# Optimization experiments

Measured on AMD Instinct MI355X. Metric: run time of the kernel, lower is better.

## Reference

```python
import jax, jax.numpy as jnp
import numpy as np

EPS = 1e-5

def layer_norm(x, g, b):
    m = jnp.mean(x, axis=-1, keepdims=True)
    v = jnp.var(x, axis=-1, keepdims=True)
    return (x - m) / jnp.sqrt(v + EPS) * g + b

def setup_inputs() -> dict:
    key = jax.random.key(0)
    B, N, D, H, F = 2, 2048, 1024, 16, 4096
    ks = jax.random.split(key, 12)
    s = 0.02
    return {
        "x": jax.random.normal(ks[0], (B, N, D), dtype=jnp.float32),
        "wq": jax.random.normal(ks[1], (D, D), dtype=jnp.float32) * s,
        "bq": jnp.zeros((D,), jnp.float32),
        "wk": jax.random.normal(ks[2], (D, D), dtype=jnp.float32) * s,
        "bk": jnp.zeros((D,), jnp.float32),
        "wv": jax.random.normal(ks[3], (D, D), dtype=jnp.float32) * s,
        "bv": jnp.zeros((D,), jnp.float32),
        "g1": jnp.ones((D,), jnp.float32),
        "b1": jnp.zeros((D,), jnp.float32),
        "g2": jnp.ones((D,), jnp.float32),
        "b2": jnp.zeros((D,), jnp.float32),
        "w1": jax.random.normal(ks[4], (D, F), dtype=jnp.float32) * s,
        "bw1": jnp.zeros((F,), jnp.float32),
        "gf": jnp.ones((F,), jnp.float32),
        "bf": jnp.zeros((F,), jnp.float32),
        "w2": jax.random.normal(ks[5], (F, D), dtype=jnp.float32) * s,
        "bw2": jnp.zeros((D,), jnp.float32),
        "num_heads": 16,
    }

def reference(x, wq, bq, wk, bk, wv, bv, g1, b1, g2, b2, w1, bw1, gf, bf, w2, bw2, num_heads):
    B, N, D = x.shape
    H = num_heads
    E = D // H
    h = layer_norm(x, g1, b1)
    q = (h @ wq + bq).reshape(B, N, H, E).transpose(0, 2, 1, 3)  # B H N E
    k = (h @ wk + bk).reshape(B, N, H, E).transpose(0, 2, 1, 3)
    v = (h @ wv + bv).reshape(B, N, H, E).transpose(0, 2, 1, 3)
    # NOTE: original scales by 1/sqrt(1/emb_dim) == sqrt(emb_dim)
    scale = jnp.sqrt(jnp.float32(D))
    score = jnp.einsum('bhne,bhme->bhnm', q, k) * scale  # B H N N
    w = jax.nn.softmax(score, axis=-1)
    attn = jnp.einsum('bhnm,bhme->bhne', w, v)
    attn = attn.transpose(0, 2, 1, 3).reshape(B, N, D)
    x = x + attn  # dropout = identity in eval
    h2 = layer_norm(x, g2, b2)
    # MLP: Linear -> (Dropout) -> LayerNorm -> ReLU -> Linear; NO residual add (faithful to source)
    u = layer_norm(h2 @ w1 + bw1, gf, bf)
    return jax.nn.relu(u) @ w2 + bw2
```

## Files before the change

### kernel.cpp

```cpp
#include <hip/hip_runtime.h>

typedef unsigned short u16;
typedef _Float16 f16;
typedef _Float16 f16x8 __attribute__((ext_vector_type(8)));
typedef float f32x4 __attribute__((ext_vector_type(4)));
typedef unsigned short u16x4 __attribute__((ext_vector_type(4)));
typedef unsigned int u32x4 __attribute__((ext_vector_type(4)));

__device__ __forceinline__ u16 f2h(float f) {
    f16 h = (f16)f;
    return *reinterpret_cast<u16*>(&h);
}
__device__ __forceinline__ float h2f(u16 u) {
    f16 h = *reinterpret_cast<f16*>(&u);
    return (float)h;
}

__device__ __forceinline__ unsigned cvtpkh(float lo, float hi) {
    unsigned r;
    asm volatile("v_cvt_pkrtz_f16_f32 %0, %1, %2" : "=v"(r) : "v"(lo), "v"(hi));
    return r;
}

__device__ __forceinline__ void gload16(const u16* g, u16* l) {
    __builtin_amdgcn_global_load_lds((const __attribute__((address_space(1))) unsigned int*)g,
                                     (__attribute__((address_space(3))) unsigned int*)l, 16, 0, 0);
}

#define RAW_BARRIER() __builtin_amdgcn_s_barrier()
#define WAITCNT_VM(N) asm volatile("s_waitcnt vmcnt(" #N ")" ::: "memory")

__global__ void transpose_cast3(const float* __restrict__ W0, u16* __restrict__ T0,
                                const float* __restrict__ W1, u16* __restrict__ T1,
                                const float* __restrict__ W2, u16* __restrict__ T2,
                                int K, int N) {
    __shared__ float t[32][33];
    const float* W = (blockIdx.z == 0) ? W0 : (blockIdx.z == 1) ? W1 : W2;
    u16* Wt = (blockIdx.z == 0) ? T0 : (blockIdx.z == 1) ? T1 : T2;
    const int n0 = blockIdx.x * 32, k0 = blockIdx.y * 32;
    const int tx = threadIdx.x, ty = threadIdx.y;
#pragma unroll
    for (int i = 0; i < 32; i += 8)
        t[ty + i][tx] = W[(size_t)(k0 + ty + i) * N + n0 + tx];
    __syncthreads();
#pragma unroll
    for (int i = 0; i < 32; i += 8)
        Wt[(size_t)(n0 + ty + i) * K + k0 + tx] = f2h(t[tx][ty + i]);
}

__global__ void transpose_cast(const float* __restrict__ W, u16* __restrict__ Wt,
                               int K, int N) {
    __shared__ float t[32][33];
    const int n0 = blockIdx.x * 32, k0 = blockIdx.y * 32;
    const int tx = threadIdx.x, ty = threadIdx.y;
#pragma unroll
    for (int i = 0; i < 32; i += 8)
        t[ty + i][tx] = W[(size_t)(k0 + ty + i) * N + n0 + tx];
    __syncthreads();
#pragma unroll
    for (int i = 0; i < 32; i += 8)
        Wt[(size_t)(n0 + ty + i) * K + k0 + tx] = f2h(t[tx][ty + i]);
}

__global__ __launch_bounds__(256) void ln_f32_f16(const float* __restrict__ in,
                                                  const float* __restrict__ g,
                                                  const float* __restrict__ b,
                                                  u16* __restrict__ out) {
    constexpr int Dl = 1024;
    const int row = blockIdx.x, tid = threadIdx.x;
    const float4 v = *(const float4*)&in[(size_t)row * Dl + tid * 4];
    const float* vp = (const float*)&v;
    float s = v.x + v.y + v.z + v.w;
    float s2 = v.x * v.x + v.y * v.y + v.z * v.z + v.w * v.w;
#pragma unroll
    for (int off = 32; off; off >>= 1) { s += __shfl_xor(s, off); s2 += __shfl_xor(s2, off); }
    __shared__ float red[8];
    const int lane = tid & 63, wid = tid >> 6;
    if (lane == 0) { red[wid] = s; red[4 + wid] = s2; }
    __syncthreads();
    s = red[0] + red[1] + red[2] + red[3];
    s2 = red[4] + red[5] + red[6] + red[7];
    const float mean = s * (1.0f / Dl);
    const float rstd = rsqrtf(s2 * (1.0f / Dl) - mean * mean + 1e-5f);
    u16x4 pk;
#pragma unroll
    for (int i = 0; i < 4; ++i) {
        const int col = tid * 4 + i;
        pk[i] = f2h((vp[i] - mean) * rstd * g[col] + b[col]);
    }
    *(u16x4*)&out[(size_t)row * Dl + tid * 4] = pk;
}

__global__ __launch_bounds__(256) void ln_relu_f16(u16* __restrict__ mid,
                                                   const float* __restrict__ g,
                                                   const float* __restrict__ b) {
    constexpr int Fl = 4096;
    const int row = blockIdx.x, tid = threadIdx.x;
    u16* rp = mid + (size_t)row * Fl;
    float v[16];
    u32x4 raw[2];
#pragma unroll
    for (int c = 0; c < 2; ++c) raw[c] = *(const u32x4*)&rp[tid * 16 + c * 8];
#pragma unroll
    for (int c = 0; c < 2; ++c)
#pragma unroll
        for (int j = 0; j < 4; ++j) {
            const unsigned u = raw[c][j];
            v[c * 8 + j * 2] = h2f((u16)(u & 0xffffu));
            v[c * 8 + j * 2 + 1] = h2f((u16)(u >> 16));
        }
    float s = 0.f, s2 = 0.f;
#pragma unroll
    for (int i = 0; i < 16; ++i) { s += v[i]; s2 += v[i] * v[i]; }
#pragma unroll
    for (int off = 32; off; off >>= 1) { s += __shfl_xor(s, off); s2 += __shfl_xor(s2, off); }
    __shared__ float red[8];
    const int lane = tid & 63, wid = tid >> 6;
    if (lane == 0) { red[wid] = s; red[4 + wid] = s2; }
    __syncthreads();
    s = red[0] + red[1] + red[2] + red[3];
    s2 = red[4] + red[5] + red[6] + red[7];
    const float mean = s * (1.0f / Fl);
    const float rstd = rsqrtf(s2 * (1.0f / Fl) - mean * mean + 1e-5f);
    unsigned w[8];
#pragma unroll
    for (int j = 0; j < 8; ++j) {
        const int col = tid * 16 + j * 2;
        const float y0 = fmaxf((v[j * 2] - mean) * rstd * g[col] + b[col], 0.f);
        const float y1 = fmaxf((v[j * 2 + 1] - mean) * rstd * g[col + 1] + b[col + 1], 0.f);
        w[j] = (unsigned)f2h(y0) | ((unsigned)f2h(y1) << 16);
    }
    *(u32x4*)&rp[tid * 16] = *(u32x4*)&w[0];
    *(u32x4*)&rp[tid * 16 + 8] = *(u32x4*)&w[4];
}

template <int EPI, int BN>
__global__ __launch_bounds__(256, 2) void gemm_f16(const u16* __restrict__ A,
                                                   const u16* __restrict__ Bt,
                                                   const float* __restrict__ bias,
                                                   u16* __restrict__ outB,
                                                   float* __restrict__ outF,
                                                   int M_, int N_, int K_) {
    constexpr int BK = 32;
    constexpr int NJ = BN / 32;
    __shared__ u16 As[2][128 * BK];
    __shared__ u16 Bs[2][BN * BK];
    const int tid = threadIdx.x;
    const int lane = tid & 63;
    const int wid = tid >> 6;
    const int m0 = blockIdx.y * 128;
    const int n0 = blockIdx.x * BN;
    const int wr = (wid >> 1) * 64;
    const int wc = (wid & 1) * (BN / 2);
    const int fr = lane & 15;
    const int fg = (lane >> 4) * 8;

    const int srow = wid * 32 + (lane >> 2);
    const int srB = wid * (BN / 4) + (lane >> 2);
    const int scol = (lane & 3) * 8;
    const u16* pa0 = A + (size_t)(m0 + srow) * K_ + scol;
    const u16* pa1 = pa0 + (size_t)16 * K_;
    const u16* pb0 = Bt + (size_t)(n0 + srB) * K_ + scol;
    const u16* pb1 = pb0 + (size_t)16 * K_;
    const int aoff = wid * 1024;
    const int boff = wid * (BN / 4) * BK;

    auto stage = [&](int k0, int buf) {
        gload16(pa0 + k0, &As[buf][aoff]);
        gload16(pa1 + k0, &As[buf][aoff + 512]);
        gload16(pb0 + k0, &Bs[buf][boff]);
        if constexpr (BN == 128) gload16(pb1 + k0, &Bs[buf][boff + 512]);
    };

    f32x4 acc[4][NJ] = {};
    const int nt = K_ / BK;

    stage(0, 0);
    WAITCNT_VM(0);
    RAW_BARRIER();

    for (int t = 0; t < nt; ++t) {
        const int buf = t & 1;
        if (t + 1 < nt) stage((t + 1) * BK, buf ^ 1);
        f16x8 aF[4], bF[NJ];
#pragma unroll
        for (int i = 0; i < 4; ++i) aF[i] = *(const f16x8*)&As[buf][(wr + i * 16 + fr) * BK + fg];
#pragma unroll
        for (int j = 0; j < NJ; ++j) bF[j] = *(const f16x8*)&Bs[buf][(wc + j * 16 + fr) * BK + fg];
#pragma unroll
        for (int i = 0; i < 4; ++i)
#pragma unroll
            for (int j = 0; j < NJ; ++j)
                acc[i][j] = __builtin_amdgcn_mfma_f32_16x16x32_f16(aF[i], bF[j], acc[i][j], 0, 0, 0);
        WAITCNT_VM(0);
        RAW_BARRIER();
    }

    const int g4 = (lane >> 4) * 4;
#pragma unroll
    for (int i = 0; i < 4; ++i) {
#pragma unroll
        for (int j = 0; j < NJ; ++j) {
            const int mb = m0 + wr + i * 16 + g4;
            const int nb = n0 + wc + j * 16 + fr;
            const float bv = bias[nb];
            if constexpr (EPI == 0) {
#pragma unroll
                for (int r = 0; r < 4; ++r)
                    outB[(size_t)(mb + r) * N_ + nb] = f2h(acc[i][j][r] + bv);
            } else {
#pragma unroll
                for (int r = 0; r < 4; ++r)
                    outF[(size_t)(mb + r) * N_ + nb] = acc[i][j][r] + bv;
            }
        }
    }
}

__global__ __launch_bounds__(256, 4) void gemm_qkv(const u16* __restrict__ A,
                                                   const u16* __restrict__ qW,
                                                   const u16* __restrict__ kW,
                                                   const u16* __restrict__ vW,
                                                   const float* __restrict__ bq,
                                                   const float* __restrict__ bk,
                                                   const float* __restrict__ bv,
                                                   u16* __restrict__ qb, u16* __restrict__ kb,
                                                   u16* __restrict__ vtb,
                                                   int M_, int K_) {
    constexpr int BK = 32;
    __shared__ u16 As[2][128 * BK];
    __shared__ u16 Bs[2][64 * BK];
    const int tid = threadIdx.x;
    const int lane = tid & 63;
    const int wid = tid >> 6;
    const int region = blockIdx.x >> 4;
    const int n0 = (blockIdx.x & 15) * 64;
    const int m0 = blockIdx.y * 128;
    const int wr = (wid >> 1) * 64;
    const int wc = (wid & 1) * 32;
    const int fr = lane & 15;
    const int fg = (lane >> 4) * 8;

    const int srow = wid * 32 + (lane >> 2);
    const int srB = wid * 16 + (lane >> 2);
    const int scol = (lane & 3) * 8;

    const u16* B = (region == 0) ? qW : (region == 1) ? kW : vW;
    const u16* pa0 = A + (size_t)(m0 + srow) * K_ + scol;
    const u16* pa1 = pa0 + (size_t)16 * K_;
    const u16* pb = B + (size_t)(n0 + srB) * K_ + scol;
    const int aoff = wid * 1024;
    const int boff = wid * 512;

    auto stage = [&](int k0, int buf) {
        gload16(pa0 + k0, &As[buf][aoff]);
        gload16(pa1 + k0, &As[buf][aoff + 512]);
        gload16(pb + k0, &Bs[buf][boff]);
    };

    f32x4 acc[4][2] = {};
    const int nt = K_ / BK;

    stage(0, 0);
    WAITCNT_VM(0);
    RAW_BARRIER();

    for (int t = 0; t < nt; ++t) {
        const int buf = t & 1;
        if (t + 1 < nt) stage((t + 1) * BK, buf ^ 1);
        f16x8 aF[4], bF[2];
#pragma unroll
        for (int i = 0; i < 4; ++i) aF[i] = *(const f16x8*)&As[buf][(wr + i * 16 + fr) * BK + fg];
#pragma unroll
        for (int j = 0; j < 2; ++j) bF[j] = *(const f16x8*)&Bs[buf][(wc + j * 16 + fr) * BK + fg];
#pragma unroll
        for (int i = 0; i < 4; ++i)
#pragma unroll
            for (int j = 0; j < 2; ++j)
                acc[i][j] = __builtin_amdgcn_mfma_f32_16x16x32_f16(aF[i], bF[j], acc[i][j], 0, 0, 0);
        WAITCNT_VM(0);
        RAW_BARRIER();
    }

    const float* bias = (region == 0) ? bq : (region == 1) ? bk : bv;
    const float scale = (region == 0) ? 32.f : 1.f;
    const int g4 = (lane >> 4) * 4;
#pragma unroll
    for (int i = 0; i < 4; ++i) {
#pragma unroll
        for (int j = 0; j < 2; ++j) {
            const int mb = m0 + wr + i * 16 + g4;
            const int nb = n0 + wc + j * 16 + fr;
            const float bv_ = bias[nb];
            const int h = nb >> 6, e = nb & 63;
            if (region < 2) {
                u16* outp = (region == 0) ? qb : kb;
#pragma unroll
                for (int r = 0; r < 4; ++r) {
                    const int m = mb + r;
                    const size_t idx = ((size_t)((m >> 11) * 16 + h) * 2048 + (m & 2047)) * 64 + e;
                    outp[idx] = f2h((acc[i][j][r] + bv_) * scale);
                }
            } else {
                const int b_ = mb >> 11, np = mb & 2047;
                u16x4 pk;
#pragma unroll
                for (int r = 0; r < 4; ++r) pk[r] = f2h(acc[i][j][r] + bv_);
                *(u16x4*)&vtb[((size_t)(b_ * 16 + h) * 64 + e) * 2048 + np] = pk;
            }
        }
    }
}

__global__ __launch_bounds__(512, 4) void attn_kernel(const u16* __restrict__ q,
                                                      const u16* __restrict__ k,
                                                      const u16* __restrict__ vt,
                                                      const float* __restrict__ x,
                                                      float* __restrict__ x2) {
    constexpr int N = 2048, E = 64, KB = 64, NT = N / KB;
    constexpr float L2E = 1.4426950408889634f;
    __shared__ u16 Ks[2][64 * 64];
    __shared__ u16 Vs[2][64 * 64];
    __shared__ unsigned Ps[8][16][36];

    const int tid = threadIdx.x;
    const int lane = tid & 63;
    const int wid = tid >> 6;
    const int bh = blockIdx.x >> 4;
    const int q0 = (blockIdx.x & 15) * 128;
    const u16* qh = q + (size_t)bh * N * E;
    const u16* kh = k + (size_t)bh * N * E;
    const u16* vh = vt + (size_t)bh * E * N;

    const int fr = lane & 15;
    const int fgrp = lane >> 4;
    const int fg8 = fgrp * 8;
    int pc[2];
#pragma unroll
    for (int ks = 0; ks < 2; ++ks) pc[ks] = 8 * (((ks << 2) + fgrp) ^ (fr & 7));

    const int srow = wid * 8 + (lane >> 3);
    const int swc = 8 * ((lane & 7) ^ (lane >> 3));
    u16* dK = &Ks[0][wid * 8 * 64];
    u16* dV = &Vs[0][wid * 8 * 64];
    constexpr int BUFO = 64 * 64;

    f16x8 qf[2];
#pragma unroll
    for (int ks = 0; ks < 2; ++ks)
        qf[ks] = *(const f16x8*)&qh[(size_t)(q0 + wid * 16 + fr) * E + ks * 32 + fg8];

    auto stage = [&](int t, int buf) {
        const size_t kb = (size_t)t * KB;
        gload16(kh + (kb + srow) * E + swc, dK + buf * BUFO);
        gload16(vh + (size_t)srow * N + kb + swc, dV + buf * BUFO);
    };

    f32x4 o[4] = {};
    float mrow = -1e30f, lpart = 0.f;

    stage(0, 0);

    for (int t = 0; t < NT; ++t) {
        const int buf = t & 1;
        RAW_BARRIER();
        if (t + 1 < NT) {
            stage(t + 1, buf ^ 1);
            WAITCNT_VM(2);
        } else {
            WAITCNT_VM(0);
        }
        RAW_BARRIER();

        const u16* KK = &Ks[buf][0];
        const u16* VV = &Vs[buf][0];

        f32x4 s[4] = {};
#pragma unroll
        for (int fn = 0; fn < 4; ++fn)
#pragma unroll
            for (int ks = 0; ks < 2; ++ks) {
                const f16x8 kf = *(const f16x8*)&KK[(fn * 16 + fr) * 64 + pc[ks]];
                s[fn] = __builtin_amdgcn_mfma_f32_16x16x32_f16(kf, qf[ks], s[fn], 0, 0, 0);
            }

        float lmax = fmaxf(fmaxf(fmaxf(s[0][0], s[0][1]), fmaxf(s[0][2], s[0][3])),
                           fmaxf(fmaxf(s[1][0], s[1][1]), fmaxf(s[1][2], s[1][3])));
        lmax = fmaxf(lmax, fmaxf(fmaxf(fmaxf(s[2][0], s[2][1]), fmaxf(s[2][2], s[2][3])),
                                 fmaxf(fmaxf(s[3][0], s[3][1]), fmaxf(s[3][2], s[3][3]))));
        if (!__all(lmax <= mrow + 8.f)) {
            float m2 = fmaxf(lmax, __shfl_xor(lmax, 16));
            m2 = fmaxf(m2, __shfl_xor(m2, 32));
            const float mnew = fmaxf(mrow, m2);
            const float fac = exp2f((mrow - mnew) * L2E);
            mrow = mnew;
            lpart *= fac;
            float fo[4];
#pragma unroll
            for (int r = 0; r < 4; ++r) fo[r] = __shfl(fac, fgrp * 4 + r);
#pragma unroll
            for (int fe = 0; fe < 4; ++fe)
#pragma unroll
                for (int r = 0; r < 4; ++r) o[fe][r] *= fo[r];
        }

        const float nml = -mrow * L2E;
#pragma unroll
        for (int fn = 0; fn < 4; ++fn) {
            const float p0 = exp2f(fmaf(s[fn][0], L2E, nml));
            const float p1 = exp2f(fmaf(s[fn][1], L2E, nml));
            const float p2 = exp2f(fmaf(s[fn][2], L2E, nml));
            const float p3 = exp2f(fmaf(s[fn][3], L2E, nml));
            lpart += (p0 + p1) + (p2 + p3);
            uint2 w;
            w.x = cvtpkh(p0, p1);
            w.y = cvtpkh(p2, p3);
            *(uint2*)&Ps[wid][fr][fn * 8 + fgrp * 2] = w;
        }

        const u16* prow = (const u16*)&Ps[wid][fr][0];
        f16x8 pf[2];
#pragma unroll
        for (int ks = 0; ks < 2; ++ks) pf[ks] = *(const f16x8*)&prow[ks * 32 + fg8];
#pragma unroll
        for (int fe = 0; fe < 4; ++fe)
#pragma unroll
            for (int ks = 0; ks < 2; ++ks) {
                const f16x8 vf = *(const f16x8*)&VV[(fe * 16 + fr) * 64 + pc[ks]];
                o[fe] = __builtin_amdgcn_mfma_f32_16x16x32_f16(pf[ks], vf, o[fe], 0, 0, 0);
            }
    }

    float lsum = lpart + __shfl_xor(lpart, 16);
    lsum += __shfl_xor(lsum, 32);
    float rl[4];
#pragma unroll
    for (int r = 0; r < 4; ++r) rl[r] = 1.0f / __shfl(lsum, fgrp * 4 + r);

    const int b_ = bh >> 4, h_ = bh & 15;
#pragma unroll
    for (int fe = 0; fe < 4; ++fe)
#pragma unroll
        for (int r = 0; r < 4; ++r) {
            const int npos = q0 + wid * 16 + fgrp * 4 + r;
            const size_t idx = ((size_t)(b_ * 2048 + npos)) * 1024 + h_ * 64 + fe * 16 + fr;
            x2[idx] = x[idx] + o[fe][r] * rl[r];
        }
}

extern "C" void kernel_launch(void* const* d_in, const int* in_sizes, int n_in,
                              void* d_out, int out_size, void* d_ws, size_t ws_size,
                              hipStream_t stream) {
    const float* x = (const float*)d_in[0];
    const float* wq = (const float*)d_in[1];
    const float* bq = (const float*)d_in[2];
    const float* wk = (const float*)d_in[3];
    const float* bk = (const float*)d_in[4];
    const float* wv = (const float*)d_in[5];
    const float* bv = (const float*)d_in[6];
    const float* g1 = (const float*)d_in[7];
    const float* b1 = (const float*)d_in[8];
    const float* g2 = (const float*)d_in[9];
    const float* b2 = (const float*)d_in[10];
    const float* w1 = (const float*)d_in[11];
    const float* bw1 = (const float*)d_in[12];
    const float* gf = (const float*)d_in[13];
    const float* bf = (const float*)d_in[14];
    const float* w2 = (const float*)d_in[15];
    const float* bw2 = (const float*)d_in[16];
    float* out = (float*)d_out;

    constexpr int Bc = 2, Nc = 2048, Dc = 1024, Fc = 4096, Mc = 4096;

    char* ws = (char*)d_ws;
    auto alloc = [&](size_t bytes) {
        char* p = ws;
        ws += (bytes + 255) & ~(size_t)255;
        return p;
    };
    u16* wqt = (u16*)alloc((size_t)Dc * Dc * 2);
    u16* wkt = (u16*)alloc((size_t)Dc * Dc * 2);
    u16* wvt = (u16*)alloc((size_t)Dc * Dc * 2);
    u16* w1t = (u16*)alloc((size_t)Dc * Fc * 2);
    u16* w2t = (u16*)alloc((size_t)Fc * Dc * 2);
    char* region = (char*)alloc((size_t)Mc * Dc * 2 * 4);
    u16* h1 = (u16*)region;
    u16* qb = h1 + (size_t)Mc * Dc;
    u16* kb = qb + (size_t)Mc * Dc;
    u16* vtb = kb + (size_t)Mc * Dc;
    u16* mid = (u16*)region;
    float* x2 = (float*)alloc((size_t)Mc * Dc * 4);
    u16* h2 = (u16*)alloc((size_t)Mc * Dc * 2);

    const dim3 tb(32, 8);
    transpose_cast3<<<dim3(Dc / 32, Dc / 32, 3), tb, 0, stream>>>(wq, wqt, wk, wkt, wv, wvt, Dc, Dc);
    transpose_cast<<<dim3(Fc / 32, Dc / 32), tb, 0, stream>>>(w1, w1t, Dc, Fc);
    transpose_cast<<<dim3(Dc / 32, Fc / 32), tb, 0, stream>>>(w2, w2t, Fc, Dc);

    ln_f32_f16<<<Mc, 256, 0, stream>>>(x, g1, b1, h1);

    gemm_qkv<<<dim3(48, Mc / 128), 256, 0, stream>>>(h1, wqt, wkt, wvt, bq, bk, bv,
                                                     qb, kb, vtb, Mc, Dc);

    attn_kernel<<<Bc * 16 * (Nc / 128), 512, 0, stream>>>(qb, kb, vtb, x, x2);

    ln_f32_f16<<<Mc, 256, 0, stream>>>(x2, g2, b2, h2);

    gemm_f16<0, 128><<<dim3(Fc / 128, Mc / 128), 256, 0, stream>>>(h2, w1t, bw1, mid, nullptr, Mc, Fc, Dc);

    ln_relu_f16<<<Mc, 256, 0, stream>>>(mid, gf, bf);

    gemm_f16<1, 64><<<dim3(Dc / 64, Mc / 128), 256, 0, stream>>>(mid, w2t, bw2, nullptr, out, Mc, Dc, Fc);
}
```

Before: 287.1 us.

## Add XCD-aware block swizzle, MFMA priority hints, and raw exp2 intrinsic

Remaps workgroup IDs in the GEMM, QKV and attention kernels so that consecutive logical tiles land on the same XCD, which is meant to improve L2 reuse of shared A/B and K/V tiles. It also raises wave priority around the MFMA loops in attention, replaces exp2f with the hardware exp2 builtin to avoid range-handling code, and drops volatile from the pack-convert asm so the compiler can schedule it. The swizzle assumes the grid size is divisible by 8, and the raw exp2 builtin may handle denormals and extreme inputs less precisely.

Result: faster. 263.8 us (-8.1%).

```diff
diff --git a/kernel.cpp b/kernel.cpp
--- a/kernel.cpp
+++ b/kernel.cpp
@@ -16,9 +16,11 @@
     return (float)h;
 }
 
+__device__ __forceinline__ float exp2v(float x) { return __builtin_amdgcn_exp2f(x); }
+
 __device__ __forceinline__ unsigned cvtpkh(float lo, float hi) {
     unsigned r;
-    asm volatile("v_cvt_pkrtz_f16_f32 %0, %1, %2" : "=v"(r) : "v"(lo), "v"(hi));
+    asm("v_cvt_pkrtz_f16_f32 %0, %1, %2" : "=v"(r) : "v"(lo), "v"(hi));
     return r;
 }
 
@@ -29,6 +31,10 @@
 
 #define RAW_BARRIER() __builtin_amdgcn_s_barrier()
 #define WAITCNT_VM(N) asm volatile("s_waitcnt vmcnt(" #N ")" ::: "memory")
+
+__device__ __forceinline__ int xcd_swz(int bid, int nwg) {
+    return (bid & 7) * (nwg >> 3) + (bid >> 3);
+}
 
 __global__ void transpose_cast3(const float* __restrict__ W0, u16* __restrict__ T0,
                                 const float* __restrict__ W1, u16* __restrict__ T1,
@@ -148,8 +154,9 @@
     const int tid = threadIdx.x;
     const int lane = tid & 63;
     const int wid = tid >> 6;
-    const int m0 = blockIdx.y * 128;
-    const int n0 = blockIdx.x * BN;
+    const int swz = xcd_swz(blockIdx.y * gridDim.x + blockIdx.x, gridDim.x * gridDim.y);
+    const int m0 = (swz / gridDim.x) * 128;
+    const int n0 = (swz % gridDim.x) * BN;
     const int wr = (wid >> 1) * 64;
     const int wc = (wid & 1) * (BN / 2);
     const int fr = lane & 15;
@@ -233,9 +240,11 @@
     const int tid = threadIdx.x;
     const int lane = tid & 63;
     const int wid = tid >> 6;
-    const int region = blockIdx.x >> 4;
-    const int n0 = (blockIdx.x & 15) * 64;
-    const int m0 = blockIdx.y * 128;
+    const int swz = xcd_swz(blockIdx.y * gridDim.x + blockIdx.x, gridDim.x * gridDim.y);
+    const int bx = swz % gridDim.x;
+    const int region = bx >> 4;
+    const int n0 = (bx & 15) * 64;
+    const int m0 = (swz / gridDim.x) * 128;
     const int wr = (wid >> 1) * 64;
     const int wc = (wid & 1) * 32;
     const int fr = lane & 15;
@@ -326,8 +335,9 @@
     const int tid = threadIdx.x;
     const int lane = tid & 63;
     const int wid = tid >> 6;
-    const int bh = blockIdx.x >> 4;
-    const int q0 = (blockIdx.x & 15) * 128;
+    const int swzb = xcd_swz(blockIdx.x, gridDim.x);
+    const int bh = swzb >> 4;
+    const int q0 = (swzb & 15) * 128;
     const u16* qh = q + (size_t)bh * N * E;
     const u16* kh = k + (size_t)bh * N * E;
     const u16* vh = vt + (size_t)bh * E * N;
@@ -376,6 +386,7 @@
         const u16* VV = &Vs[buf][0];
 
         f32x4 s[4] = {};
+        __builtin_amdgcn_s_setprio(1);
 #pragma unroll
         for (int fn = 0; fn < 4; ++fn)
 #pragma unroll
@@ -383,6 +394,7 @@
                 const f16x8 kf = *(const f16x8*)&KK[(fn * 16 + fr) * 64 + pc[ks]];
                 s[fn] = __builtin_amdgcn_mfma_f32_16x16x32_f16(kf, qf[ks], s[fn], 0, 0, 0);
             }
+        __builtin_amdgcn_s_setprio(0);
 
         float lmax = fmaxf(fmaxf(fmaxf(s[0][0], s[0][1]), fmaxf(s[0][2], s[0][3])),
                            fmaxf(fmaxf(s[1][0], s[1][1]), fmaxf(s[1][2], s[1][3])));
@@ -392,7 +404,7 @@
             float m2 = fmaxf(lmax, __shfl_xor(lmax, 16));
             m2 = fmaxf(m2, __shfl_xor(m2, 32));
             const float mnew = fmaxf(mrow, m2);
-            const float fac = exp2f((mrow - mnew) * L2E);
+            const float fac = exp2v((mrow - mnew) * L2E);
             mrow = mnew;
             lpart *= fac;
             float fo[4];
@@ -407,10 +419,10 @@
         const float nml = -mrow * L2E;
 #pragma unroll
         for (int fn = 0; fn < 4; ++fn) {
-            const float p0 = exp2f(fmaf(s[fn][0], L2E, nml));
-            const float p1 = exp2f(fmaf(s[fn][1], L2E, nml));
-            const float p2 = exp2f(fmaf(s[fn][2], L2E, nml));
-            const float p3 = exp2f(fmaf(s[fn][3], L2E, nml));
+            const float p0 = exp2v(fmaf(s[fn][0], L2E, nml));
+            const float p1 = exp2v(fmaf(s[fn][1], L2E, nml));
+            const float p2 = exp2v(fmaf(s[fn][2], L2E, nml));
+            const float p3 = exp2v(fmaf(s[fn][3], L2E, nml));
             lpart += (p0 + p1) + (p2 + p3);
             uint2 w;
             w.x = cvtpkh(p0, p1);
@@ -422,6 +434,7 @@
         f16x8 pf[2];
 #pragma unroll
         for (int ks = 0; ks < 2; ++ks) pf[ks] = *(const f16x8*)&prow[ks * 32 + fg8];
+        __builtin_amdgcn_s_setprio(1);
 #pragma unroll
         for (int fe = 0; fe < 4; ++fe)
 #pragma unroll
@@ -429,6 +442,7 @@
                 const f16x8 vf = *(const f16x8*)&VV[(fe * 16 + fr) * 64 + pc[ks]];
                 o[fe] = __builtin_amdgcn_mfma_f32_16x16x32_f16(pf[ks], vf, o[fe], 0, 0, 0);
             }
+        __builtin_amdgcn_s_setprio(0);
     }
 
     float lsum = lpart + __shfl_xor(lpart, 16);
```
